# Performance work log

Hardware: AMD Instinct MI355X
Metric: run time of the kernel (lower is better)

The kernel has to match this reference:

```python
import jax, jax.numpy as jnp
import numpy as np

N_KG, N, E, R, H, D_OUT = 50000, 20000, 320000, 8, 4, 64
IN_CH = 256  # 128 kg_emb + 128 ccle projection
HD = H * D_OUT  # 256


def setup_inputs() -> dict:
    key = jax.random.key(0)
    ks = jax.random.split(key, 16)
    nrm = lambda k, shape, s=0.05: jax.random.normal(k, shape, dtype=jnp.float32) * s
    return {
        "kg_emb": nrm(ks[0], (N_KG, 128), 1.0),
        "ccle": nrm(ks[1], (N_KG, 4), 1.0),
        "node_id": jax.random.randint(ks[2], (N,), 0, N_KG),
        "edge_index": jax.random.randint(ks[3], (2, E), 0, N),
        "edge_type": jax.random.randint(ks[4], (E,), 0, R),
        "ccle_w1": nrm(ks[5], (4, 32)), "ccle_b1": jnp.zeros((32,), jnp.float32),
        "ccle_w2": nrm(ks[6], (32, 128)), "ccle_b2": jnp.zeros((128,), jnp.float32),
        "w1": nrm(ks[7], (R, IN_CH, HD)),
        "q1": nrm(ks[8], (HD, H)), "k1": nrm(ks[9], (HD, H)),
        "bias1": jnp.zeros((HD,), jnp.float32),
        "w2": nrm(ks[10], (R, HD, HD)),
        "q2": nrm(ks[11], (HD, H)), "k2": nrm(ks[12], (HD, H)),
        "bias2": jnp.zeros((HD,), jnp.float32),
        "skip_w1": nrm(ks[13], (IN_CH, 256)), "skip_b1": jnp.zeros((256,), jnp.float32),
        "skip_w2": nrm(ks[14], (256, 256)), "skip_b2": jnp.zeros((256,), jnp.float32),
    }


def _segment_softmax(logits, segs, n):
    # numerically stable softmax over variable-size dst-neighborhoods
    m = jax.lax.stop_gradient(jax.ops.segment_max(logits, segs, num_segments=n))
    m = jnp.where(jnp.isfinite(m), m, 0.0)
    e = jnp.exp(logits - m[segs])
    s = jax.ops.segment_sum(e, segs, num_segments=n)
    return e / jnp.maximum(s[segs], 1e-16)


def _rgat(x, edge_index, edge_type, w, q, k, bias, n):
    # PyG RGATConv: additive-self-attention, across-relation, dim=1, concat=True
    # per-relation node transform then per-edge gather == x_e @ w[edge_type]
    xw = jnp.einsum('nd,rdo->rno', x, w)              # [R, N, H*D]
    src, dst = edge_index[0], edge_index[1]
    outj = xw[edge_type, src]                          # [E, H*D] source feats
    outi = xw[edge_type, dst]                          # [E, H*D] target feats
    alpha = jax.nn.leaky_relu(outi @ q + outj @ k, 0.2)  # [E, H]
    alpha = _segment_softmax(alpha, dst, n)
    msg = (outj.reshape(-1, H, D_OUT) * alpha[:, :, None]).reshape(-1, HD)
    return jax.ops.segment_sum(msg, dst, num_segments=n) + bias


def reference(kg_emb, ccle, ccle_w1, ccle_b1, ccle_w2, ccle_b2,
              w1, q1, k1, bias1, w2, q2, k2, bias2,
              skip_w1, skip_b1, skip_w2, skip_b2,
              node_id, edge_index, edge_type):
    lrelu = lambda v: jax.nn.leaky_relu(v, 0.01)  # nn.LeakyReLU default slope
    ccle_out = lrelu(ccle @ ccle_w1 + ccle_b1) @ ccle_w2 + ccle_b2
    x_in = jnp.concatenate([kg_emb[node_id], ccle_out[node_id]], axis=1)  # [N, 256]
    n = x_in.shape[0]
    x = lrelu(_rgat(x_in, edge_index, edge_type, w1, q1, k1, bias1, n))
    # dropout is identity in eval mode
    x = _rgat(x, edge_index, edge_type, w2, q2, k2, bias2, n)
    skip = lrelu(x_in @ skip_w1 + skip_b1) @ skip_w2 + skip_b2
    return lrelu(x + skip)
```

## Files before the change

### kernel.cpp

```cpp
#include <hip/hip_runtime.h>
#include <hip/hip_bf16.h>

typedef __bf16 bf16x8 __attribute__((ext_vector_type(8)));
typedef float  f32x4  __attribute__((ext_vector_type(4)));
typedef float  v2f    __attribute__((ext_vector_type(2)));

__device__ __forceinline__ void async_cp16(const __bf16* g, __bf16* l) {
    __builtin_amdgcn_global_load_lds(
        (const __attribute__((address_space(1))) void*)g,
        (__attribute__((address_space(3))) void*)l, 16, 0, 0);
}

__global__ __launch_bounds__(256) void preamble_kernel(
    const float* __restrict__ kg_emb, const float* __restrict__ ccle,
    const float* __restrict__ cw1, const float* __restrict__ cb1,
    const float* __restrict__ cw2, const float* __restrict__ cb2,
    const int* __restrict__ node_id, __bf16* __restrict__ x_in, int Nn,
    const float* __restrict__ w1, const float* __restrict__ w2,
    const float* __restrict__ sw1, const float* __restrict__ sw2,
    __bf16* __restrict__ w1t, __bf16* __restrict__ w2t,
    __bf16* __restrict__ sw1t, __bf16* __restrict__ sw2t, int R,
    const float* __restrict__ q1, const float* __restrict__ k1,
    const float* __restrict__ q2, const float* __restrict__ k2,
    __bf16* __restrict__ wqkT1, __bf16* __restrict__ wqkT2,
    const int* __restrict__ ei, int* __restrict__ deg, int E,
    int nTrans, int nWqk, int nBx)
{
    __shared__ __align__(16) char sraw[8448];
    const int bid = blockIdx.x;
    const int t = threadIdx.x;

    if (bid < nTrans) {
        __bf16 (*tile)[65] = (__bf16 (*)[65])sraw;
        int zr = bid >> 4, rem = bid & 15;
        int kb = (rem & 3) * 64, nb = (rem >> 2) * 64;
        const float* B; __bf16* Bt;
        if (zr < R)           { B = w1 + (size_t)zr * 65536;       Bt = w1t + (size_t)zr * 65536; }
        else if (zr < 2 * R)  { B = w2 + (size_t)(zr - R) * 65536; Bt = w2t + (size_t)(zr - R) * 65536; }
        else if (zr == 2 * R) { B = sw1;                            Bt = sw1t; }
        else                  { B = sw2;                            Bt = sw2t; }
        for (int idx = t; idx < 4096; idx += 256) {
            int rr = idx >> 6, cc = idx & 63;
            tile[rr][cc] = (__bf16)B[(kb + rr) * 256 + nb + cc];
        }
        __syncthreads();
        for (int idx = t; idx < 4096; idx += 256) {
            int rr = idx >> 6, cc = idx & 63;
            Bt[(nb + rr) * 256 + kb + cc] = tile[cc][rr];
        }
    } else if (bid < nTrans + nWqk) {
        float* qs = (float*)sraw;
        float* ks = qs + 1024;
        int wb = bid - nTrans;
        int zz = wb >> 3, ib = wb & 7;
        int r = zz % R;
        const float* w = (zz < R) ? w1 : w2;
        const float* q = (zz < R) ? q1 : q2;
        const float* k = (zz < R) ? k1 : k2;
        __bf16* wqkT = (zz < R) ? wqkT1 : wqkT2;
        for (int i = t; i < 1024; i += 256) { qs[i] = q[i]; ks[i] = k[i]; }
        __syncthreads();
        int inl = t >> 3, g = t & 7;
        const float* wr = w + (size_t)r * 65536;
        int in = ib * 32 + inl;
        float pq0=0,pq1=0,pq2=0,pq3=0, pk0=0,pk1=0,pk2=0,pk3=0;
        const float* row = wr + in * 256 + g * 32;
        #pragma unroll 8
        for (int oj = 0; oj < 32; oj++) {
            float wv = row[oj];
            int out = g * 32 + oj;
            pq0 += wv * qs[out*4+0]; pq1 += wv * qs[out*4+1];
            pq2 += wv * qs[out*4+2]; pq3 += wv * qs[out*4+3];
            pk0 += wv * ks[out*4+0]; pk1 += wv * ks[out*4+1];
            pk2 += wv * ks[out*4+2]; pk3 += wv * ks[out*4+3];
        }
        #pragma unroll
        for (int d = 4; d >= 1; d >>= 1) {
            pq0 += __shfl_down(pq0, d, 64); pq1 += __shfl_down(pq1, d, 64);
            pq2 += __shfl_down(pq2, d, 64); pq3 += __shfl_down(pq3, d, 64);
            pk0 += __shfl_down(pk0, d, 64); pk1 += __shfl_down(pk1, d, 64);
            pk2 += __shfl_down(pk2, d, 64); pk3 += __shfl_down(pk3, d, 64);
        }
        if (g == 0) {
            wqkT[(r*8+0)*256 + in] = (__bf16)pq0; wqkT[(r*8+1)*256 + in] = (__bf16)pq1;
            wqkT[(r*8+2)*256 + in] = (__bf16)pq2; wqkT[(r*8+3)*256 + in] = (__bf16)pq3;
            wqkT[(r*8+4)*256 + in] = (__bf16)pk0; wqkT[(r*8+5)*256 + in] = (__bf16)pk1;
            wqkT[(r*8+6)*256 + in] = (__bf16)pk2; wqkT[(r*8+7)*256 + in] = (__bf16)pk3;
        }
    } else if (bid < nTrans + nWqk + nBx) {
        float (*h)[32] = (float (*)[32])sraw;
        int bb = bid - nTrans - nWqk;
        int sub = t >> 7;
        int tt  = t & 127;
        int i   = bb * 2 + sub;
        if (i < Nn && tt < 32) {
            int kid = node_id[i];
            float a = 0.f;
            #pragma unroll
            for (int j = 0; j < 4; j++) a += ccle[kid*4 + j] * cw1[j*32 + tt];
            a += cb1[tt];
            h[sub][tt] = a < 0.f ? 0.01f * a : a;
        }
        __syncthreads();
        if (i < Nn) {
            int kid = node_id[i];
            x_in[i*256 + tt] = (__bf16)kg_emb[kid*128 + tt];
            float a = 0.f;
            #pragma unroll
            for (int j = 0; j < 32; j++) a += h[sub][j] * cw2[j*128 + tt];
            a += cb2[tt];
            x_in[i*256 + 128 + tt] = (__bf16)a;
        }
    } else {
        int e = (bid - nTrans - nWqk - nBx) * 256 + t;
        if (e < E) atomicAdd(&deg[ei[E + e]], 1);
    }
}

__global__ __launch_bounds__(1024) void scan_kernel(
    const int* __restrict__ deg, int* __restrict__ row_off, int* __restrict__ cursor, int Nn)
{
    __shared__ int wsum[16];
    __shared__ int carry_s;
    int t = threadIdx.x;
    int lane = t & 63, wid = t >> 6;
    if (t == 0) carry_s = 0;
    __syncthreads();
    for (int base = 0; base < Nn; base += 4096) {
        int i0 = base + t * 4;
        int4 v = make_int4(0, 0, 0, 0);
        if (i0 + 3 < Nn) v = *(const int4*)(deg + i0);
        else if (i0 < Nn) {
            v.x = deg[i0];
            if (i0 + 1 < Nn) v.y = deg[i0 + 1];
            if (i0 + 2 < Nn) v.z = deg[i0 + 2];
        }
        int s = v.x + v.y + v.z + v.w;
        int incl = s;
        #pragma unroll
        for (int off = 1; off < 64; off <<= 1) {
            int x = __shfl_up(incl, off, 64);
            if (lane >= off) incl += x;
        }
        if (lane == 63) wsum[wid] = incl;
        __syncthreads();
        if (wid == 0) {
            int wv = (lane < 16) ? wsum[lane] : 0;
            #pragma unroll
            for (int off = 1; off < 16; off <<= 1) {
                int x = __shfl_up(wv, off, 64);
                if (lane >= off) wv += x;
            }
            if (lane < 16) wsum[lane] = wv;
        }
        __syncthreads();
        int wprefix = (wid > 0) ? wsum[wid - 1] : 0;
        int e0 = carry_s + wprefix + incl - s;
        int e1 = e0 + v.x, e2 = e1 + v.y, e3 = e2 + v.z;
        if (i0 + 3 < Nn) {
            *(int4*)(row_off + i0) = make_int4(e0, e1, e2, e3);
            *(int4*)(cursor + i0)  = make_int4(e0, e1, e2, e3);
        } else if (i0 < Nn) {
            row_off[i0] = e0; cursor[i0] = e0;
            if (i0 + 1 < Nn) { row_off[i0+1] = e1; cursor[i0+1] = e1; }
            if (i0 + 2 < Nn) { row_off[i0+2] = e2; cursor[i0+2] = e2; }
        }
        __syncthreads();
        if (t == 1023) carry_s += wsum[15];
        __syncthreads();
    }
    if (t == 0) row_off[Nn] = carry_s;
}

__global__ void scatter_kernel(const int* __restrict__ ei, const int* __restrict__ et,
                               int* __restrict__ cursor, int* __restrict__ cidx, int E) {
    int e = blockIdx.x * 256 + threadIdx.x;
    if (e < E) {
        int d = ei[E + e];
        int pos = atomicAdd(&cursor[d], 1);
        cidx[pos] = (et[e] << 20) | ei[e];
    }
}

__global__ __launch_bounds__(256, 3) void gemm_lds_kernel(
    const __bf16* __restrict__ A, const __bf16* __restrict__ Askip,
    const __bf16* __restrict__ Bt, long bStride, const __bf16* __restrict__ Bskip,
    const __bf16* __restrict__ wqkT,
    unsigned char* __restrict__ C8, long cStride,
    __bf16* __restrict__ Cskip, const float* __restrict__ biasSkip, float slopeSkip,
    float* __restrict__ s_qk,
    int M, int R2, int mb)
{
    __shared__ __bf16 sm[2][8192];
    const int R2m = R2 + 3;
    const int id = blockIdx.x;
    const int xcd = id & 7, slot = id >> 3;
    const int g = xcd + 8 * (slot / R2m);
    const int member = slot % R2m;
    if (g >= mb) return;
    const bool isSqk  = (member == R2 + 2);
    const bool isSkip = (member >= R2) && !isSqk;
    const int m0 = g * 128;
    const int n0 = isSkip ? (member - R2) * 128 : ((member < R2) ? (member & 1) * 128 : 0);
    const int z = (member < R2) ? (member >> 1) : 0;
    const __bf16* __restrict__ Ab = isSkip ? Askip : A;
    const __bf16* __restrict__ Bb = isSqk ? wqkT : (isSkip ? Bskip : (Bt + (long)z * bStride));

    const int t = threadIdx.x;
    const int wave = t >> 6, lane = t & 63;
    const int wy = (wave >> 1) * 64, wx = (wave & 1) * 64;
    const int lr = lane & 15, lq = lane >> 4;

    int c0 = wave * 128 + lane;
    int row0 = c0 >> 2, kq0 = ((c0 & 3) ^ ((row0 >> 1) & 3));
    int c1 = c0 + 64;
    int row1 = c1 >> 2, kq1 = ((c1 & 3) ^ ((row1 >> 1) & 3));
    int ar0 = m0 + row0; if (ar0 >= M) ar0 = M - 1;
    int ar1 = m0 + row1; if (ar1 >= M) ar1 = M - 1;
    const long a_g0 = (long)ar0 * 256 + kq0 * 8;
    const long a_g1 = (long)ar1 * 256 + kq1 * 8;
    const long b_g0 = (long)(n0 + row0) * 256 + kq0 * 8;
    const long b_g1 = (long)(n0 + row1) * 256 + kq1 * 8;
    const int lds_w0 = (wave * 128) * 8, lds_w1 = (wave * 128 + 64) * 8;

    int a_lds[4], b_lds[4];
    #pragma unroll
    for (int tm = 0; tm < 4; tm++) {
        int row = wy + tm * 16 + lr;
        a_lds[tm] = (row * 4 + (lq ^ ((row >> 1) & 3))) * 8;
    }
    #pragma unroll
    for (int tn = 0; tn < 4; tn++) {
        int row = wx + tn * 16 + lr;
        b_lds[tn] = 4096 + (row * 4 + (lq ^ ((row >> 1) & 3))) * 8;
    }

    f32x4 acc[4][4];
    #pragma unroll
    for (int a_ = 0; a_ < 4; a_++)
        #pragma unroll
        for (int b_ = 0; b_ < 4; b_++) acc[a_][b_] = (f32x4){0.f, 0.f, 0.f, 0.f};

    async_cp16(Ab + a_g0, &sm[0][lds_w0]);
    async_cp16(Ab + a_g1, &sm[0][lds_w1]);
    async_cp16(Bb + b_g0, &sm[0][4096 + lds_w0]);
    async_cp16(Bb + b_g1, &sm[0][4096 + lds_w1]);

    #pragma unroll
    for (int it = 0; it < 8; it++) {
        const int cur = it & 1;
        __syncthreads();
        if (it < 7) {
            const int k0 = (it + 1) * 32;
            async_cp16(Ab + a_g0 + k0, &sm[cur ^ 1][lds_w0]);
            async_cp16(Ab + a_g1 + k0, &sm[cur ^ 1][lds_w1]);
            async_cp16(Bb + b_g0 + k0, &sm[cur ^ 1][4096 + lds_w0]);
            async_cp16(Bb + b_g1 + k0, &sm[cur ^ 1][4096 + lds_w1]);
        }
        bf16x8 af[4], bfr[4];
        #pragma unroll
        for (int tm = 0; tm < 4; tm++) af[tm]  = *(const bf16x8*)(&sm[cur][a_lds[tm]]);
        #pragma unroll
        for (int tn = 0; tn < 4; tn++) bfr[tn] = *(const bf16x8*)(&sm[cur][b_lds[tn]]);
        #pragma unroll
        for (int tm = 0; tm < 4; tm++)
            #pragma unroll
            for (int tn = 0; tn < 4; tn++)
                acc[tm][tn] = __builtin_amdgcn_mfma_f32_16x16x32_bf16(af[tm], bfr[tn], acc[tm][tn], 0, 0, 0);
    }

    if (isSqk) {
        if (wx == 0) {
            #pragma unroll
            for (int tm = 0; tm < 4; tm++) {
                #pragma unroll
                for (int tn = 0; tn < 4; tn++) {
                    int col = tn * 16 + lr;
                    #pragma unroll
                    for (int ii = 0; ii < 4; ii++) {
                        int rg = m0 + wy + tm * 16 + lq * 4 + ii;
                        if (rg < M) s_qk[(long)rg * 64 + col] = acc[tm][tn][ii];
                    }
                }
            }
        }
    } else if (isSkip) {
        #pragma unroll
        for (int tm = 0; tm < 4; tm++) {
            #pragma unroll
            for (int tn = 0; tn < 4; tn++) {
                int col = n0 + wx + tn * 16 + lr;
                float bcol = biasSkip[col];
                #pragma unroll
                for (int ii = 0; ii < 4; ii++) {
                    int rg = m0 + wy + tm * 16 + lq * 4 + ii;
                    if (rg < M) {
                        float v = acc[tm][tn][ii] + bcol;
                        v = v < 0.f ? v * slopeSkip : v;
                        Cskip[(long)rg * 256 + col] = (__bf16)v;
                    }
                }
            }
        }
    } else {
        unsigned char* __restrict__ Cb = C8 + (long)z * cStride;
        #pragma unroll
        for (int tm = 0; tm < 4; tm++) {
            #pragma unroll
            for (int tn = 0; tn < 4; tn++) {
                int col = n0 + wx + tn * 16 + lr;
                #pragma unroll
                for (int ii = 0; ii < 4; ii++) {
                    int rg = m0 + wy + tm * 16 + lq * 4 + ii;
                    if (rg < M) {
                        float v = acc[tm][tn][ii];
                        int pk = __builtin_amdgcn_cvt_pk_fp8_f32(v, v, 0, false);
                        Cb[(long)rg * 256 + col] = (unsigned char)(pk & 0xFF);
                    }
                }
            }
        }
    }
}

__global__ __launch_bounds__(256) void agg_kernel(
    const unsigned char* __restrict__ XW8, const float* __restrict__ s_qk,
    const int* __restrict__ row_off, const int* __restrict__ cidx,
    const float* __restrict__ bias, const __bf16* __restrict__ skipb,
    __bf16* __restrict__ outb, float* __restrict__ outf, float slope, int Nn)
{
    int lane = threadIdx.x & 63;
    int i = blockIdx.x * 4 + (threadIdx.x >> 6);
    if (i >= Nn) return;
    int base = row_off[i];
    int deg = row_off[i + 1] - base;

    int half = lane >> 5;
    int l32 = lane & 31;
    int myh = l32 >> 3;
    int d8 = l32 * 8;

    float4 bv0 = *(const float4*)(bias + d8);
    float4 bv1 = *(const float4*)(bias + d8 + 4);
    uint4 skq = make_uint4(0u, 0u, 0u, 0u);
    if (skipb) skq = *(const uint4*)(skipb + (long)i * 256 + d8);

    float acc[8];
    #pragma unroll
    for (int u = 0; u < 8; u++) acc[u] = 0.f;
    float ss0 = 0.f, ss1 = 0.f, ss2 = 0.f, ss3 = 0.f;

    for (int c0 = 0; c0 < deg; c0 += 64) {
        int e = c0 + lane;
        int cc = 0;
        if (e < deg) cc = cidx[base + e];
        int cnt = min(64, deg - c0);

        uint2 xv[8];
        #pragma unroll
        for (int u = 0; u < 8; u++) {
            int cj = __shfl(cc, u * 2 + half, 64);
            int src = cj & 0xFFFFF, et = cj >> 20;
            xv[u] = *(const uint2*)(XW8 + ((long)et * Nn + src) * 256 + d8);
        }

        float p0 = 0.f, p1 = 0.f, p2 = 0.f, p3 = 0.f;
        if (e < deg) {
            int src = cc & 0xFFFFF, et = cc >> 20;
            float4 sqv = *(const float4*)(s_qk + (long)i * 64 + et * 8);
            float4 skv = *(const float4*)(s_qk + (long)src * 64 + et * 8 + 4);
            float l0 = sqv.x + skv.x; l0 = l0 < 0.f ? 0.2f * l0 : l0;
            float l1 = sqv.y + skv.y; l1 = l1 < 0.f ? 0.2f * l1 : l1;
            float l2 = sqv.z + skv.z; l2 = l2 < 0.f ? 0.2f * l2 : l2;
            float l3 = sqv.w + skv.w; l3 = l3 < 0.f ? 0.2f * l3 : l3;
            p0 = __expf(fminf(l0, 40.f)); p1 = __expf(fminf(l1, 40.f));
            p2 = __expf(fminf(l2, 40.f)); p3 = __expf(fminf(l3, 40.f));
        }
        ss0 += p0; ss1 += p1; ss2 += p2; ss3 += p3;

        for (int j0 = 0; j0 < cnt; j0 += 16) {
            uint2 xvn[8];
            const bool more = (j0 + 16 < cnt);
            if (more) {
                #pragma unroll
                for (int u = 0; u < 8; u++) {
                    int cj = __shfl(cc, j0 + 16 + u * 2 + half, 64);
                    int src = cj & 0xFFFFF, et = cj >> 20;
                    xvn[u] = *(const uint2*)(XW8 + ((long)et * Nn + src) * 256 + d8);
                }
            }
            #pragma unroll
            for (int u = 0; u < 8; u++) {
                int srcl = j0 + u * 2 + half;
                float q0 = __shfl(p0, srcl, 64);
                float q1 = __shfl(p1, srcl, 64);
                float q2 = __shfl(p2, srcl, 64);
                float q3 = __shfl(p3, srcl, 64);
                float w = (myh & 2) ? ((myh & 1) ? q3 : q2) : ((myh & 1) ? q1 : q0);
                uint2 xvu = xv[u];
                v2f f0 = __builtin_amdgcn_cvt_pk_f32_fp8(xvu.x, false);
                v2f f1 = __builtin_amdgcn_cvt_pk_f32_fp8(xvu.x, true);
                v2f f2 = __builtin_amdgcn_cvt_pk_f32_fp8(xvu.y, false);
                v2f f3 = __builtin_amdgcn_cvt_pk_f32_fp8(xvu.y, true);
                acc[0] += w * f0.x; acc[1] += w * f0.y;
                acc[2] += w * f1.x; acc[3] += w * f1.y;
                acc[4] += w * f2.x; acc[5] += w * f2.y;
                acc[6] += w * f3.x; acc[7] += w * f3.y;
            }
            if (more) {
                #pragma unroll
                for (int u = 0; u < 8; u++) xv[u] = xvn[u];
            }
        }
    }
    #pragma unroll
    for (int u = 0; u < 8; u++) acc[u] += __shfl_xor(acc[u], 32, 64);
    #pragma unroll
    for (int off = 32; off >= 1; off >>= 1) {
        ss0 += __shfl_xor(ss0, off, 64);
        ss1 += __shfl_xor(ss1, off, 64);
        ss2 += __shfl_xor(ss2, off, 64);
        ss3 += __shfl_xor(ss3, off, 64);
    }
    float ssh = (myh & 2) ? ((myh & 1) ? ss3 : ss2) : ((myh & 1) ? ss1 : ss0);
    float inv = 1.f / fmaxf(ssh, 1e-16f);

    float barr[8] = { bv0.x, bv0.y, bv0.z, bv0.w, bv1.x, bv1.y, bv1.z, bv1.w };
    const __bf16* skp = (const __bf16*)&skq;
    float vout[8];
    #pragma unroll
    for (int u = 0; u < 8; u++) {
        float v = acc[u] * inv + barr[u];
        if (skipb) v += (float)skp[u];
        vout[u] = v < 0.f ? slope * v : v;
    }
    if (outb) {
        if (half == 0) {
            __bf16 tmp[8];
            #pragma unroll
            for (int u = 0; u < 8; u++) tmp[u] = (__bf16)vout[u];
            *(uint4*)(outb + (long)i * 256 + d8) = *(const uint4*)tmp;
        }
    } else {
        float4 f4;
        if (half == 0) { f4 = make_float4(vout[0], vout[1], vout[2], vout[3]);
                         *(float4*)(outf + (long)i * 256 + d8) = f4; }
        else           { f4 = make_float4(vout[4], vout[5], vout[6], vout[7]);
                         *(float4*)(outf + (long)i * 256 + d8 + 4) = f4; }
    }
}

extern "C" void kernel_launch(void* const* d_in, const int* in_sizes, int n_in,
                              void* d_out, int out_size, void* d_ws, size_t ws_size,
                              hipStream_t stream)
{
    const float* kg_emb  = (const float*)d_in[0];
    const float* ccle    = (const float*)d_in[1];
    const int*   node_id = (const int*)d_in[2];
    const int*   edge_ix = (const int*)d_in[3];
    const int*   edge_ty = (const int*)d_in[4];
    const float* ccle_w1 = (const float*)d_in[5];
    const float* ccle_b1 = (const float*)d_in[6];
    const float* ccle_w2 = (const float*)d_in[7];
    const float* ccle_b2 = (const float*)d_in[8];
    const float* w1      = (const float*)d_in[9];
    const float* q1      = (const float*)d_in[10];
    const float* k1      = (const float*)d_in[11];
    const float* bias1   = (const float*)d_in[12];
    const float* w2      = (const float*)d_in[13];
    const float* q2      = (const float*)d_in[14];
    const float* k2      = (const float*)d_in[15];
    const float* bias2   = (const float*)d_in[16];
    const float* skip_w1 = (const float*)d_in[17];
    const float* skip_b1 = (const float*)d_in[18];
    const float* skip_w2 = (const float*)d_in[19];
    const float* skip_b2 = (const float*)d_in[20];

    const int Nn = in_sizes[2];
    const int E  = in_sizes[4];
    const int R  = in_sizes[9] / (256 * 256);

    char* p = (char*)d_ws;
    auto alloc = [&](size_t bytes) { char* r = p; p += (bytes + 255) & ~(size_t)255; return r; };
    __bf16* x_in  = (__bf16*)alloc((size_t)Nn * 256 * 2);
    __bf16* x1    = (__bf16*)alloc((size_t)Nn * 256 * 2);
    __bf16* sh    = (__bf16*)alloc((size_t)Nn * 256 * 2);
    __bf16* skipb = (__bf16*)alloc((size_t)Nn * 256 * 2);
    unsigned char* XW8 = (unsigned char*)alloc((size_t)R * Nn * 256);
    float*  s_qk  = (float*)alloc((size_t)Nn * 64 * 4);
    __bf16* wqkT1 = (__bf16*)alloc((size_t)64 * 256 * 2);
    __bf16* wqkT2 = (__bf16*)alloc((size_t)64 * 256 * 2);
    __bf16* w1t   = (__bf16*)alloc((size_t)R * 65536 * 2);
    __bf16* w2t   = (__bf16*)alloc((size_t)R * 65536 * 2);
    __bf16* sw1t  = (__bf16*)alloc((size_t)65536 * 2);
    __bf16* sw2t  = (__bf16*)alloc((size_t)65536 * 2);
    int* deg     = (int*)alloc((size_t)Nn * 4);
    int* row_off = (int*)alloc((size_t)(Nn + 1) * 4);
    int* cursor  = (int*)alloc((size_t)Nn * 4);
    int* cidx    = (int*)alloc((size_t)E * 4);

    const int mb = (Nn + 127) / 128;
    const int eb = (E + 255) / 256;
    const int grp = (mb + 7) / 8;
    const int R2 = 2 * R;
    const int gemm_blocks = 8 * grp * (R2 + 3);

    const int nTrans = 16 * (2 * R + 2);
    const int nWqk   = 2 * R * 8;
    const int nBx    = (Nn + 1) / 2;
    const int pre_blocks = nTrans + nWqk + nBx + eb;

    (void)hipMemsetAsync(deg, 0, (size_t)Nn * 4, stream);
    preamble_kernel<<<dim3(pre_blocks), 256, 0, stream>>>(
        kg_emb, ccle, ccle_w1, ccle_b1, ccle_w2, ccle_b2, node_id, x_in, Nn,
        w1, w2, skip_w1, skip_w2, w1t, w2t, sw1t, sw2t, R,
        q1, k1, q2, k2, wqkT1, wqkT2,
        edge_ix, deg, E, nTrans, nWqk, nBx);
    scan_kernel<<<dim3(1), 1024, 0, stream>>>(deg, row_off, cursor, Nn);
    scatter_kernel<<<dim3(eb), 256, 0, stream>>>(edge_ix, edge_ty, cursor, cidx, E);

    gemm_lds_kernel<<<dim3(gemm_blocks), 256, 0, stream>>>(
        x_in, x_in, w1t, 65536L, sw1t, wqkT1, XW8, (long)Nn * 256, sh, skip_b1, 0.01f,
        s_qk, Nn, R2, mb);
    agg_kernel<<<dim3((Nn + 3) / 4), 256, 0, stream>>>(
        XW8, s_qk, row_off, cidx, bias1, nullptr, x1, nullptr, 0.01f, Nn);

    gemm_lds_kernel<<<dim3(gemm_blocks), 256, 0, stream>>>(
        x1, sh, w2t, 65536L, sw2t, wqkT2, XW8, (long)Nn * 256, skipb, skip_b2, 1.0f,
        s_qk, Nn, R2, mb);
    agg_kernel<<<dim3((Nn + 3) / 4), 256, 0, stream>>>(
        XW8, s_qk, row_off, cidx, bias2, skipb, nullptr, (float*)d_out, 0.01f, Nn);
}
```

Measured before the change: 331.7 us.

## Fold edge scatter into GEMM1 launch and overlap layer-2 skip GEMM with aggregation

After: 328.5 us. Within noise of the previous version (-1.0%).

```diff
diff --git a/kernel.cpp b/kernel.cpp
--- a/kernel.cpp
+++ b/kernel.cpp
@@ -172,16 +172,6 @@
     if (t == 0) row_off[Nn] = carry_s;
 }
 
-__global__ void scatter_kernel(const int* __restrict__ ei, const int* __restrict__ et,
-                               int* __restrict__ cursor, int* __restrict__ cidx, int E) {
-    int e = blockIdx.x * 256 + threadIdx.x;
-    if (e < E) {
-        int d = ei[E + e];
-        int pos = atomicAdd(&cursor[d], 1);
-        cidx[pos] = (et[e] << 20) | ei[e];
-    }
-}
-
 __global__ __launch_bounds__(256, 3) void gemm_lds_kernel(
     const __bf16* __restrict__ A, const __bf16* __restrict__ Askip,
     const __bf16* __restrict__ Bt, long bStride, const __bf16* __restrict__ Bskip,
@@ -189,17 +179,27 @@
     unsigned char* __restrict__ C8, long cStride,
     __bf16* __restrict__ Cskip, const float* __restrict__ biasSkip, float slopeSkip,
     float* __restrict__ s_qk,
-    int M, int R2, int mb)
+    int M, int R2, int mb, int nMem, int hasSkip,
+    const int* __restrict__ ei, const int* __restrict__ et,
+    int* __restrict__ cursor, int* __restrict__ cidx, int E, int nGemm)
 {
     __shared__ __bf16 sm[2][8192];
-    const int R2m = R2 + 3;
     const int id = blockIdx.x;
+    if (id >= nGemm) {
+        int e = (id - nGemm) * 256 + threadIdx.x;
+        if (e < E) {
+            int d = ei[E + e];
+            int pos = atomicAdd(&cursor[d], 1);
+            cidx[pos] = (et[e] << 20) | ei[e];
+        }
+        return;
+    }
     const int xcd = id & 7, slot = id >> 3;
-    const int g = xcd + 8 * (slot / R2m);
-    const int member = slot % R2m;
+    const int g = xcd + 8 * (slot / nMem);
+    const int member = slot % nMem;
     if (g >= mb) return;
-    const bool isSqk  = (member == R2 + 2);
-    const bool isSkip = (member >= R2) && !isSqk;
+    const bool isSqk  = (member == nMem - 1);
+    const bool isSkip = hasSkip && !isSqk && (member >= R2);
     const int m0 = g * 128;
     const int n0 = isSkip ? (member - R2) * 128 : ((member < R2) ? (member & 1) * 128 : 0);
     const int z = (member < R2) ? (member >> 1) : 0;
@@ -320,6 +320,203 @@
                 }
             }
         }
+    }
+}
+
+__global__ __launch_bounds__(256) void agg_skip_kernel(
+    const unsigned char* __restrict__ XW8, const float* __restrict__ s_qk,
+    const int* __restrict__ row_off, const int* __restrict__ cidx,
+    const float* __restrict__ bias, __bf16* __restrict__ outb, float slope, int Nn,
+    const __bf16* __restrict__ Ask, const __bf16* __restrict__ Bsk,
+    __bf16* __restrict__ Csk, const float* __restrict__ biasSk, int nSkip)
+{
+    extern __shared__ __bf16 smx[];
+    if ((int)blockIdx.x < nSkip) {
+        const int sb = blockIdx.x;
+        const int m0 = (sb >> 1) * 128;
+        const int n0 = (sb & 1) * 128;
+        const int t = threadIdx.x;
+        const int wave = t >> 6, lane = t & 63;
+        const int wy = (wave >> 1) * 64, wx = (wave & 1) * 64;
+        const int lr = lane & 15, lq = lane >> 4;
+
+        int c0 = wave * 128 + lane;
+        int row0 = c0 >> 2, kq0 = ((c0 & 3) ^ ((row0 >> 1) & 3));
+        int c1 = c0 + 64;
+        int row1 = c1 >> 2, kq1 = ((c1 & 3) ^ ((row1 >> 1) & 3));
+        int ar0 = m0 + row0; if (ar0 >= Nn) ar0 = Nn - 1;
+        int ar1 = m0 + row1; if (ar1 >= Nn) ar1 = Nn - 1;
+        const long a_g0 = (long)ar0 * 256 + kq0 * 8;
+        const long a_g1 = (long)ar1 * 256 + kq1 * 8;
+        const long b_g0 = (long)(n0 + row0) * 256 + kq0 * 8;
+        const long b_g1 = (long)(n0 + row1) * 256 + kq1 * 8;
+        const int lds_w0 = (wave * 128) * 8, lds_w1 = (wave * 128 + 64) * 8;
+
+        int a_lds[4], b_lds[4];
+        #pragma unroll
+        for (int tm = 0; tm < 4; tm++) {
+            int row = wy + tm * 16 + lr;
+            a_lds[tm] = (row * 4 + (lq ^ ((row >> 1) & 3))) * 8;
+        }
+        #pragma unroll
+        for (int tn = 0; tn < 4; tn++) {
+            int row = wx + tn * 16 + lr;
+            b_lds[tn] = 4096 + (row * 4 + (lq ^ ((row >> 1) & 3))) * 8;
+        }
+
+        f32x4 acc[4][4];
+        #pragma unroll
+        for (int a_ = 0; a_ < 4; a_++)
+            #pragma unroll
+            for (int b_ = 0; b_ < 4; b_++) acc[a_][b_] = (f32x4){0.f, 0.f, 0.f, 0.f};
+
+        async_cp16(Ask + a_g0, &smx[lds_w0]);
+        async_cp16(Ask + a_g1, &smx[lds_w1]);
+        async_cp16(Bsk + b_g0, &smx[4096 + lds_w0]);
+        async_cp16(Bsk + b_g1, &smx[4096 + lds_w1]);
+
+        #pragma unroll
+        for (int it = 0; it < 8; it++) {
+            const int cur = it & 1;
+            __syncthreads();
+            if (it < 7) {
+                const int k0 = (it + 1) * 32;
+                async_cp16(Ask + a_g0 + k0, &smx[(cur ^ 1) * 8192 + lds_w0]);
+                async_cp16(Ask + a_g1 + k0, &smx[(cur ^ 1) * 8192 + lds_w1]);
+                async_cp16(Bsk + b_g0 + k0, &smx[(cur ^ 1) * 8192 + 4096 + lds_w0]);
+                async_cp16(Bsk + b_g1 + k0, &smx[(cur ^ 1) * 8192 + 4096 + lds_w1]);
+            }
+            bf16x8 af[4], bfr[4];
+            #pragma unroll
+            for (int tm = 0; tm < 4; tm++) af[tm]  = *(const bf16x8*)(&smx[cur * 8192 + a_lds[tm]]);
+            #pragma unroll
+            for (int tn = 0; tn < 4; tn++) bfr[tn] = *(const bf16x8*)(&smx[cur * 8192 + b_lds[tn]]);
+            #pragma unroll
+            for (int tm = 0; tm < 4; tm++)
+                #pragma unroll
+                for (int tn = 0; tn < 4; tn++)
+                    acc[tm][tn] = __builtin_amdgcn_mfma_f32_16x16x32_bf16(af[tm], bfr[tn], acc[tm][tn], 0, 0, 0);
+        }
+
+        #pragma unroll
+        for (int tm = 0; tm < 4; tm++) {
+            #pragma unroll
+            for (int tn = 0; tn < 4; tn++) {
+                int col = n0 + wx + tn * 16 + lr;
+                float bcol = biasSk[col];
+                #pragma unroll
+                for (int ii = 0; ii < 4; ii++) {
+                    int rg = m0 + wy + tm * 16 + lq * 4 + ii;
+                    if (rg < Nn) Csk[(long)rg * 256 + col] = (__bf16)(acc[tm][tn][ii] + bcol);
+                }
+            }
+        }
+        return;
+    }
+
+    int lane = threadIdx.x & 63;
+    int i = ((int)blockIdx.x - nSkip) * 4 + (threadIdx.x >> 6);
+    if (i >= Nn) return;
+    int base = row_off[i];
+    int deg = row_off[i + 1] - base;
+
+    int half = lane >> 5;
+    int l32 = lane & 31;
+    int myh = l32 >> 3;
+    int d8 = l32 * 8;
+
+    float4 bv0 = *(const float4*)(bias + d8);
+    float4 bv1 = *(const float4*)(bias + d8 + 4);
+
+    float acc[8];
+    #pragma unroll
+    for (int u = 0; u < 8; u++) acc[u] = 0.f;
+    float ss0 = 0.f, ss1 = 0.f, ss2 = 0.f, ss3 = 0.f;
+
+    for (int c0 = 0; c0 < deg; c0 += 64) {
+        int e = c0 + lane;
+        int cc = 0;
+        if (e < deg) cc = cidx[base + e];
+        int cnt = min(64, deg - c0);
+
+        uint2 xv[8];
+        #pragma unroll
+        for (int u = 0; u < 8; u++) {
+            int cj = __shfl(cc, u * 2 + half, 64);
+            int src = cj & 0xFFFFF, et = cj >> 20;
+            xv[u] = *(const uint2*)(XW8 + ((long)et * Nn + src) * 256 + d8);
+        }
+
+        float p0 = 0.f, p1 = 0.f, p2 = 0.f, p3 = 0.f;
+        if (e < deg) {
+            int src = cc & 0xFFFFF, et = cc >> 20;
+            float4 sqv = *(const float4*)(s_qk + (long)i * 64 + et * 8);
+            float4 skv = *(const float4*)(s_qk + (long)src * 64 + et * 8 + 4);
+            float l0 = sqv.x + skv.x; l0 = l0 < 0.f ? 0.2f * l0 : l0;
+            float l1 = sqv.y + skv.y; l1 = l1 < 0.f ? 0.2f * l1 : l1;
+            float l2 = sqv.z + skv.z; l2 = l2 < 0.f ? 0.2f * l2 : l2;
+            float l3 = sqv.w + skv.w; l3 = l3 < 0.f ? 0.2f * l3 : l3;
+            p0 = __expf(fminf(l0, 40.f)); p1 = __expf(fminf(l1, 40.f));
+            p2 = __expf(fminf(l2, 40.f)); p3 = __expf(fminf(l3, 40.f));
+        }
+        ss0 += p0; ss1 += p1; ss2 += p2; ss3 += p3;
+
+        for (int j0 = 0; j0 < cnt; j0 += 16) {
+            uint2 xvn[8];
+            const bool more = (j0 + 16 < cnt);
+            if (more) {
+                #pragma unroll
+                for (int u = 0; u < 8; u++) {
+                    int cj = __shfl(cc, j0 + 16 + u * 2 + half, 64);
+                    int src = cj & 0xFFFFF, et = cj >> 20;
+                    xvn[u] = *(const uint2*)(XW8 + ((long)et * Nn + src) * 256 + d8);
+                }
+            }
+            #pragma unroll
+            for (int u = 0; u < 8; u++) {
+                int srcl = j0 + u * 2 + half;
+                float q0 = __shfl(p0, srcl, 64);
+                float q1 = __shfl(p1, srcl, 64);
+                float q2 = __shfl(p2, srcl, 64);
+                float q3 = __shfl(p3, srcl, 64);
+                float w = (myh & 2) ? ((myh & 1) ? q3 : q2) : ((myh & 1) ? q1 : q0);
+                uint2 xvu = xv[u];
+                v2f f0 = __builtin_amdgcn_cvt_pk_f32_fp8(xvu.x, false);
+                v2f f1 = __builtin_amdgcn_cvt_pk_f32_fp8(xvu.x, true);
+                v2f f2 = __builtin_amdgcn_cvt_pk_f32_fp8(xvu.y, false);
+                v2f f3 = __builtin_amdgcn_cvt_pk_f32_fp8(xvu.y, true);
+                acc[0] += w * f0.x; acc[1] += w * f0.y;
+                acc[2] += w * f1.x; acc[3] += w * f1.y;
+                acc[4] += w * f2.x; acc[5] += w * f2.y;
+                acc[6] += w * f3.x; acc[7] += w * f3.y;
+            }
+            if (more) {
+                #pragma unroll
+                for (int u = 0; u < 8; u++) xv[u] = xvn[u];
+            }
+        }
+    }
+    #pragma unroll
+    for (int u = 0; u < 8; u++) acc[u] += __shfl_xor(acc[u], 32, 64);
+    #pragma unroll
+    for (int off = 32; off >= 1; off >>= 1) {
+        ss0 += __shfl_xor(ss0, off, 64);
+        ss1 += __shfl_xor(ss1, off, 64);
+        ss2 += __shfl_xor(ss2, off, 64);
+        ss3 += __shfl_xor(ss3, off, 64);
+    }
+    float ssh = (myh & 2) ? ((myh & 1) ? ss3 : ss2) : ((myh & 1) ? ss1 : ss0);
+    float inv = 1.f / fmaxf(ssh, 1e-16f);
+
+    float barr[8] = { bv0.x, bv0.y, bv0.z, bv0.w, bv1.x, bv1.y, bv1.z, bv1.w };
+    if (half == 0) {
+        __bf16 tmp[8];
+        #pragma unroll
+        for (int u = 0; u < 8; u++) {
+            float v = acc[u] * inv + barr[u];
+            tmp[u] = (__bf16)(v < 0.f ? slope * v : v);
+        }
+        *(uint4*)(outb + (long)i * 256 + d8) = *(const uint4*)tmp;
     }
 }
 
@@ -503,12 +700,14 @@
     const int eb = (E + 255) / 256;
     const int grp = (mb + 7) / 8;
     const int R2 = 2 * R;
-    const int gemm_blocks = 8 * grp * (R2 + 3);
+    const int gemm1_blocks = 8 * grp * (R2 + 3);
+    const int gemm2_blocks = 8 * grp * (R2 + 1);
 
     const int nTrans = 16 * (2 * R + 2);
     const int nWqk   = 2 * R * 8;
     const int nBx    = (Nn + 1) / 2;
     const int pre_blocks = nTrans + nWqk + nBx + eb;
+    const int nSkip2 = 2 * mb;
 
     (void)hipMemsetAsync(deg, 0, (size_t)Nn * 4, stream);
     preamble_kernel<<<dim3(pre_blocks), 256, 0, stream>>>(
@@ -517,17 +716,21 @@
         q1, k1, q2, k2, wqkT1, wqkT2,
         edge_ix, deg, E, nTrans, nWqk, nBx);
     scan_kernel<<<dim3(1), 1024, 0, stream>>>(deg, row_off, cursor, Nn);
-    scatter_kernel<<<dim3(eb), 256, 0, stream>>>(edge_ix, edge_ty, cursor, cidx, E);
-
-    gemm_lds_kernel<<<dim3(gemm_blocks), 256, 0, stream>>>(
+
+    gemm_lds_kernel<<<dim3(gemm1_blocks + eb), 256, 0, stream>>>(
         x_in, x_in, w1t, 65536L, sw1t, wqkT1, XW8, (long)Nn * 256, sh, skip_b1, 0.01f,
-        s_qk, Nn, R2, mb);
-    agg_kernel<<<dim3((Nn + 3) / 4), 256, 0, stream>>>(
-        XW8, s_qk, row_off, cidx, bias1, nullptr, x1, nullptr, 0.01f, Nn);
-
-    gemm_lds_kernel<<<dim3(gemm_blocks), 256, 0, stream>>>(
-        x1, sh, w2t, 65536L, sw2t, wqkT2, XW8, (long)Nn * 256, skipb, skip_b2, 1.0f,
-        s_qk, Nn, R2, mb);
+        s_qk, Nn, R2, mb, R2 + 3, 1,
+        edge_ix, edge_ty, cursor, cidx, E, gemm1_blocks);
+
+    agg_skip_kernel<<<dim3(nSkip2 + (Nn + 3) / 4), 256, 32768, stream>>>(
+        XW8, s_qk, row_off, cidx, bias1, x1, 0.01f, Nn,
+        sh, sw2t, skipb, skip_b2, nSkip2);
+
+    gemm_lds_kernel<<<dim3(gemm2_blocks), 256, 0, stream>>>(
+        x1, x1, w2t, 65536L, sw2t, wqkT2, XW8, (long)Nn * 256, skipb, skip_b2, 1.0f,
+        s_qk, Nn, R2, mb, R2 + 1, 0,
+        edge_ix, edge_ty, cursor, cidx, E, gemm2_blocks);
+
     agg_kernel<<<dim3((Nn + 3) / 4), 256, 0, stream>>>(
         XW8, s_qk, row_off, cidx, bias2, skipb, nullptr, (float*)d_out, 0.01f, Nn);
 }
```
